# Performance work log

Hardware: AMD Instinct MI355X
Metric: run time of the kernel (lower is better)

## Reference

```python
import jax, jax.numpy as jnp
import numpy as np

B, T, D, V, M, K = 16, 4096, 512, 32000, 256, 3
OPERATOR_RANK = 8
COVERAGE_FLOOR = 0.05
LN_EPS = 1e-5


def _causal_conv(h, w, b):
    # h: [B,T,D] -> NCH layout, left-pad K-1 for causality (matches F.pad((pad,0)))
    x = h.transpose(0, 2, 1)
    k = w.shape[-1]
    y = jax.lax.conv_general_dilated(x, w, (1,), [(k - 1, 0)],
                                     dimension_numbers=('NCH', 'OIH', 'NCH'))
    return (y + b[None, :, None]).transpose(0, 2, 1)


def _layernorm(x, g, b):
    mu = x.mean(-1, keepdims=True)
    var = ((x - mu) ** 2).mean(-1, keepdims=True)
    return (x - mu) * jax.lax.rsqrt(var + LN_EPS) * g + b


def _masked_median(vals, mask):
    # torch .median() on n valid elems = sorted[(n-1)//2] (lower median)
    valid = mask > 0.5
    cnt = valid.sum(-1)  # [B]
    s = jnp.sort(jnp.where(valid, vals, jnp.inf), axis=-1)
    idx = jnp.maximum((cnt - 1) // 2, 0).astype(jnp.int32)
    med = jnp.take_along_axis(s, idx[:, None], axis=-1)  # [B,1]
    return jnp.where(cnt[:, None] > 0, med, 0.0)


def setup_inputs() -> dict:
    key = jax.random.key(0)
    ks = jax.random.split(key, 10)
    return {
        'prompt_content_units': jax.random.randint(ks[0], (B, T), 0, V),
        'prompt_duration_obs': jax.random.uniform(ks[1], (B, T), minval=0.01, maxval=1.0),
        'prompt_mask': (jax.random.uniform(ks[2], (B, T)) < 0.9).astype(jnp.float32),
        'emb': jax.random.normal(ks[3], (V, D)) * 0.02,
        'proj_w': jax.random.normal(ks[4], (D, 4)) * 0.1,
        'proj_b': jnp.zeros((D,)),
        'conv1_w': jax.random.normal(ks[5], (D, D, K)) * 0.02,
        'conv1_b': jnp.zeros((D,)),
        'conv2_w': jax.random.normal(ks[6], (D, D, K)) * 0.02,
        'conv2_b': jnp.zeros((D,)),
        'ln_g': jnp.ones((D,)),
        'ln_b': jnp.zeros((D,)),
        'role_key': jax.random.normal(ks[7], (M, D)) * 0.02,
    }


def reference(prompt_content_units, prompt_duration_obs, prompt_mask,
              emb, proj_w, proj_b, conv1_w, conv1_b, conv2_w, conv2_b,
              ln_g, ln_b, role_key):
    mask = jnp.clip(prompt_mask, 0.0, 1.0)                       # [B,T]
    logdur = jnp.log(jnp.maximum(prompt_duration_obs, 1e-4)) * mask
    z = jnp.zeros_like(logdur)
    aux = jnp.stack([logdur, z, z, z], axis=-1)                  # [B,T,4]
    hidden = emb[prompt_content_units] + aux @ proj_w.T + proj_b # [B,T,D]
    hidden = jax.nn.gelu(_causal_conv(hidden, conv1_w, conv1_b), approximate=False)
    hidden = jax.nn.gelu(_causal_conv(hidden, conv2_w, conv2_b), approximate=False)
    hidden = _layernorm(hidden, ln_g, ln_b) * mask[..., None]

    score = jnp.einsum('btd,md->btm', hidden, role_key) / jnp.sqrt(jnp.float32(D))
    score = jnp.where(mask[..., None] <= 0.0, -10000.0, score)
    attn = jax.nn.softmax(score, axis=-1) * mask[..., None]      # [B,T,M]

    support = jnp.maximum(mask.sum(1, keepdims=True), 1.0)       # [B,1]
    global_rate = _masked_median(logdur, mask)                   # [B,1]
    ref_residual = (logdur - global_rate) * mask                 # [B,T]

    coverage = jnp.maximum(attn.sum(1), 1e-6)                    # [B,M]
    role_value = jnp.einsum('btm,bt->bm', attn, ref_residual) / coverage
    diff2 = (ref_residual[..., None] - role_value[:, None, :]) ** 2
    role_var = jnp.maximum((attn * diff2).sum(1) / coverage, 1e-4)
    role_cov = jnp.maximum(coverage / support, COVERAGE_FLOOR)
    prompt_role_fit = jnp.einsum('btm,bm->bt', attn, role_value) * mask
    zero_operator = jnp.zeros((mask.shape[0], OPERATOR_RANK), dtype=prompt_duration_obs.dtype)

    return (global_rate, zero_operator, role_value, role_var, role_cov,
            mask, logdur, ref_residual, attn, prompt_role_fit)
```

## Files before the change

### kernel.cpp

```cpp
#include <hip/hip_runtime.h>
#include <math.h>
#include <stdint.h>

#define B_  16
#define T_  4096
#define D_  512
#define M_  256
#define TP_ 4098

static constexpr long O_RATE = 0;
static constexpr long O_ZOP  = 16;
static constexpr long O_RVAL = 144;
static constexpr long O_RVAR = 4240;
static constexpr long O_RCOV = 8336;
static constexpr long O_MASK = 12432;
static constexpr long O_LOGD = 77968;
static constexpr long O_RESID= 143504;
static constexpr long O_ATTN = 209040;
static constexpr long O_FIT  = 16986256;

typedef unsigned short u16;
typedef unsigned int u32;
typedef __attribute__((ext_vector_type(8))) __bf16 bf16x8;
typedef __attribute__((ext_vector_type(4))) float fx4;

__device__ __forceinline__ float b2f(u16 u){ union{float f;uint32_t i;}v; v.i=((uint32_t)u)<<16; return v.f; }
__device__ __forceinline__ u16 f2b(float f){ union{float f;uint32_t i;}v; v.f=f; uint32_t r=v.i+0x7fffu+((v.i>>16)&1u); return (u16)(r>>16); }
__device__ __forceinline__ float clip01(float x){ return fminf(fmaxf(x, 0.f), 1.f); }
__device__ __forceinline__ float gelu_f(float x){ return 0.5f*x*(1.0f+erff(x*0.70710678118654752440f)); }

__device__ __forceinline__ void cp16(const u16* g, u16* l){
  __builtin_amdgcn_global_load_lds((__attribute__((address_space(1))) void*)g,
                                   (__attribute__((address_space(3))) void*)l, 16, 0, 0);
}


__global__ void k_init(u16* __restrict__ h0, u16* __restrict__ hA, int Cloc,
                       float* __restrict__ out){
  int i = blockIdx.x*256 + threadIdx.x;
  int nA = Cloc << 7;
  if (i < nA){
    int lb = i >> 7, r = i & 127, g = r >> 1, t = r & 1;
    *(uint4*)(h0 + ((long)(lb*64 + g)*TP_ + t)*8) = make_uint4(0,0,0,0);
  } else if (i < nA + 2048){
    int j = i - nA;
    int b = j >> 7, r = j & 127, g = r >> 1, t = r & 1;
    *(uint4*)(hA + ((long)(b*64 + g)*TP_ + t)*8) = make_uint4(0,0,0,0);
  } else if (i < nA + 2048 + 128){
    out[O_ZOP + (i - nA - 2048)] = 0.f;
  }
}

__global__ void k_repack(const float* __restrict__ w1, const float* __restrict__ w2,
                         const float* __restrict__ rk, const float* __restrict__ lng,
                         u16* __restrict__ wrp2, u16* __restrict__ rkb){
  int i = blockIdx.x*256 + threadIdx.x;
  if (i < 1572864){
    int gi = i >> 3, c7 = i & 7;
    int row = gi & 511;
    int g   = (gi >> 9) & 3;
    int kt  = (gi >> 11) & 15;
    int tg  = gi >> 15;
    int conv = tg / 3, tap = tg % 3;
    int ic = kt*32 + g*8 + c7;
    const float* w = conv ? w2 : w1;
    wrp2[i] = f2b(w[(row*512 + ic)*3 + tap]);
  } else {
    int j = i - 1572864;
    int gi = j >> 3, c7 = j & 7;
    int n  = gi & 255;
    int g  = (gi >> 8) & 3;
    int kt = gi >> 10;
    int k  = kt*32 + g*8 + c7;
    rkb[j] = f2b(rk[n*512 + k] * lng[k]);
  }
}

__global__ __launch_bounds__(64) void k_gbb(const float* __restrict__ rk,
                                            const float* __restrict__ lng,
                                            const float* __restrict__ lnb,
                                            float* __restrict__ GB,
                                            float* __restrict__ BeB){
  int n = blockIdx.x, lane = threadIdx.x;
  float sg = 0.f, sb = 0.f;
  #pragma unroll
  for (int j = 0; j < 8; ++j){
    int k = lane*8 + j;
    float kv = rk[(long)n*512 + k];
    sg += lng[k]*kv; sb += lnb[k]*kv;
  }
  #pragma unroll
  for (int d=1; d<64; d<<=1){ sg += __shfl_xor(sg, d); sb += __shfl_xor(sb, d); }
  if (lane == 0){ GB[n] = sg; BeB[n] = sb; }
}

__global__ __launch_bounds__(1024) void k_median(
    const float* __restrict__ dur, const float* __restrict__ msk,
    float* __restrict__ out, float* __restrict__ supp_f){
  __shared__ u32 keys[4096];
  __shared__ u32 hist[2048];
  __shared__ float sred[1024];
  __shared__ u32 selBin, selRank;
  __shared__ float sMed;
  const int tid = threadIdx.x;
  const int b = blockIdx.x;
  float msum = 0.f;
  for (int i = tid; i < 4096; i += 1024){
    int bt = (b << 12) + i;
    float m  = clip01(msk[bt]);
    float ld = logf(fmaxf(dur[bt], 1e-4f)) * m;
    out[O_MASK + bt] = m;
    out[O_LOGD + bt] = ld;
    u32 u = __float_as_uint(ld);
    u32 k = (u & 0x80000000u) ? ~u : (u | 0x80000000u);
    keys[i] = (m > 0.5f) ? k : 0xFFFFFFFFu;
    msum += m;
  }
  sred[tid] = msum;
  __syncthreads();
  for (int s = 512; s > 0; s >>= 1){
    if (tid < s) sred[tid] += sred[tid + s];
    __syncthreads();
  }
  float msumT = sred[0];
  int cnt = (int)(msumT + 0.5f);
  u32 prefix = 0;
  u32 r = (cnt > 0) ? (u32)((cnt - 1) >> 1) : 0u;
  if (cnt > 0){
    #pragma unroll
    for (int p = 0; p < 3; ++p){
      const int shift = (p==0) ? 21 : (p==1) ? 10 : 0;
      const int nb = (p==2) ? 1024 : 2048;
      const u32 himask = (p==0) ? 0u : (0xFFFFFFFFu << (shift + ((p==2)?10:11)));
      hist[tid] = 0u; hist[tid + 1024] = 0u;
      __syncthreads();
      for (int i = tid; i < 4096; i += 1024){
        u32 k = keys[i];
        if ((k & himask) == prefix)
          atomicAdd(&hist[(k >> shift) & (u32)(nb-1)], 1u);
      }
      __syncthreads();
      if (tid < 64){
        u32 lane = tid;
        u32 cum = 0;
        for (int chunk = 0; chunk < nb/64; ++chunk){
          u32 v = hist[chunk*64 + lane];
          u32 incl = v;
          #pragma unroll
          for (int d = 1; d < 64; d <<= 1){
            u32 o = __shfl_up(incl, d);
            if (lane >= (u32)d) incl += o;
          }
          u32 total = __shfl(incl, 63);
          if (r < cum + total){
            u32 excl = incl - v;
            bool hit = (r >= cum + excl) && (r < cum + excl + v);
            unsigned long long bal = __ballot(hit);
            int L = __ffsll((unsigned long long)bal) - 1;
            u32 exclL = __shfl(excl, L);
            if (lane == 0){ selBin = (u32)(chunk*64 + L); selRank = r - (cum + exclL); }
            break;
          }
          cum += total;
        }
      }
      __syncthreads();
      prefix |= (selBin << shift);
      r = selRank;
      __syncthreads();
    }
  }
  if (tid == 0){
    float med = 0.f;
    if (cnt > 0){
      u32 k = prefix;
      u32 u = (k & 0x80000000u) ? (k ^ 0x80000000u) : ~k;
      med = __uint_as_float(u);
    }
    out[O_RATE + b] = med;
    supp_f[b] = fmaxf(msumT, 1.0f);
    sMed = med;
  }
  __syncthreads();
  float med = sMed;
  for (int i = tid; i < 4096; i += 1024){
    int bt = (b << 12) + i;
    float m  = clip01(msk[bt]);
    float ld = logf(fmaxf(dur[bt], 1e-4f)) * m;
    out[O_RESID + bt] = (ld - med) * m;
  }
}

__global__ __launch_bounds__(256) void k_embed(
    const int* __restrict__ units, const float* __restrict__ dur,
    const float* __restrict__ msk, const float* __restrict__ emb,
    const float* __restrict__ pw, const float* __restrict__ pb,
    u16* __restrict__ h0, int b0){
  int wid = threadIdx.x >> 6, lane = threadIdx.x & 63;
  int w = blockIdx.x*4 + wid;
  int tb = w & 63, g = (w >> 6) & 63, lb = w >> 12;
  int t = tb*64 + lane;
  int bt = ((b0 + lb) << 12) + t;
  float m = clip01(msk[bt]);
  float ld = logf(fmaxf(dur[bt], 1e-4f)) * m;
  long u = units[bt];
  const float* er = emb + u*512 + g*8;
  float4 e0 = *(const float4*)er;
  float4 e1 = *(const float4*)(er + 4);
  float x[8] = {e0.x,e0.y,e0.z,e0.w,e1.x,e1.y,e1.z,e1.w};
  union { u16 s[8]; uint4 v; } o;
  #pragma unroll
  for (int j=0;j<8;++j)
    o.s[j] = f2b(x[j] + ld*pw[(g*8+j)*4] + pb[g*8+j]);
  *(uint4*)(h0 + ((long)(lb*64 + g)*TP_ + 2 + t)*8) = o.v;
}

__device__ __forceinline__ void stageA(u16* smem, const u16* hin, long aG, int t0,
                                       int tid, int kt, int base){
  { int s = tid;
    int gl = s / 258, row = s - gl*258;
    cp16(hin + (aG + (long)(kt*4 + gl)*TP_ + t0 + row)*8, &smem[(base + s)*8]); }
  if (tid < 8){
    int s = 1024 + tid;
    cp16(hin + (aG + (long)(kt*4 + 3)*TP_ + t0 + (s - 774))*8, &smem[(base + s)*8]);
  }
}
__device__ __forceinline__ void stageB(u16* smem, const u16* w, int n0,
                                       int tid, int kt, int base){
  #pragma unroll
  for (int q = 0; q < 3; ++q){
    int s2 = q*1024 + tid;
    int tap = s2 >> 10, g = (s2 >> 8) & 3, col = s2 & 255;
    cp16(w + ((long)((tap*16 + kt)*4 + g)*512 + n0 + col)*8, &smem[(base + s2)*8]);
  }
}

template<int STATS>
__global__ __launch_bounds__(1024, 4) void k_conv(const u16* __restrict__ hin,
                                                  const u16* __restrict__ wrp2c,
                                                  const float* __restrict__ bias,
                                                  u16* __restrict__ hout,
                                                  float* __restrict__ rsum,
                                                  float* __restrict__ rsumsq,
                                                  int statsBase, int nwg){
  __shared__ __align__(16) u16 smem[65664];
  const int tid = threadIdx.x;
  const int lane = tid & 63, wid = tid >> 6;
  const int wm = wid >> 2, wn = wid & 3;
  const int g4 = lane >> 4, r16 = lane & 15;
  const int cpx = nwg >> 3;
  const int wg  = ((int)blockIdx.x & 7)*cpx + ((int)blockIdx.x >> 3);
  const int nt = wg & 1, mt = wg >> 1;
  const int lb = mt >> 4, t0 = (mt & 15) << 8;
  const int n0 = nt << 8;
  const long aG = (long)lb*64*TP_;

  fx4 acc[4][4];
  #pragma unroll
  for (int i=0;i<4;++i)
    #pragma unroll
    for (int j=0;j<4;++j){ acc[i][j][0]=0.f; acc[i][j][1]=0.f; acc[i][j][2]=0.f; acc[i][j][3]=0.f; }

  stageB(smem, wrp2c, n0, tid, 0, 2064);
  stageA(smem, hin, aG, t0, tid, 0, 0);

  int cur = 0;
  #pragma unroll 1
  for (int kt = 0; kt < 16; ++kt){
    if (kt < 15){
      stageB(smem, wrp2c, n0, tid, kt+1, 2064 + (cur^1)*3072);
      stageA(smem, hin, aG, t0, tid, kt+1, (cur^1)*1032);
      asm volatile("s_waitcnt vmcnt(4)" ::: "memory");
    } else {
      asm volatile("s_waitcnt vmcnt(0)" ::: "memory");
    }
    __builtin_amdgcn_s_barrier();
    __builtin_amdgcn_sched_barrier(0);
    {
      const u16* Ab = &smem[cur*1032*8];
      const u16* Bb = &smem[(2064 + cur*3072)*8];
      #pragma unroll
      for (int tap = 0; tap < 3; ++tap){
        bf16x8 af[4], bf[4];
        #pragma unroll
        for (int mi=0;mi<4;++mi)
          af[mi] = *(const bf16x8*)&Ab[(g4*258 + wm*64 + mi*16 + r16 + tap)*8];
        #pragma unroll
        for (int ni=0;ni<4;++ni)
          bf[ni] = *(const bf16x8*)&Bb[(tap*1024 + g4*256 + wn*64 + ni*16 + r16)*8];
        __builtin_amdgcn_s_setprio(1);
        #pragma unroll
        for (int mi=0;mi<4;++mi)
          #pragma unroll
          for (int ni=0;ni<4;++ni)
            acc[mi][ni] = __builtin_amdgcn_mfma_f32_16x16x32_bf16(af[mi], bf[ni], acc[mi][ni], 0,0,0);
        __builtin_amdgcn_s_setprio(0);
      }
    }
    __builtin_amdgcn_sched_barrier(0);
    __builtin_amdgcn_s_barrier();
    cur ^= 1;
  }

  __builtin_amdgcn_sched_barrier(0);
  const int cl = r16;
  float bv[4];
  #pragma unroll
  for (int ni=0;ni<4;++ni) bv[ni] = bias[n0 + wn*64 + ni*16 + cl];
  #pragma unroll
  for (int mi=0;mi<4;++mi)
    #pragma unroll
    for (int rg=0;rg<4;++rg){
      int r = wm*64 + mi*16 + g4*4 + rg;
      float sv = 0.f, sv2 = 0.f;
      #pragma unroll
      for (int ni=0;ni<4;++ni){
        float v = gelu_f(acc[mi][ni][rg] + bv[ni]);
        int c = wn*64 + ni*16 + cl;
        smem[(c >> 3)*2048 + r*8 + (c & 7)] = f2b(v);
        if (STATS){ sv += v; sv2 += v*v; }
      }
      if (STATS){
        #pragma unroll
        for (int d=1; d<16; d<<=1){ sv += __shfl_xor(sv, d); sv2 += __shfl_xor(sv2, d); }
        if (cl == 0){
          int grow = statsBase + lb*4096 + t0 + r;
          atomicAdd(&rsum[grow], sv);
          atomicAdd(&rsumsq[grow], sv2);
        }
      }
    }
  __syncthreads();
  #pragma unroll
  for (int it = 0; it < 8; ++it){
    int s = it*1024 + tid;
    int gc = s >> 8, row = s & 255;
    long gran = aG + (long)(nt*32 + gc)*TP_ + 2 + t0 + row;
    *(uint4*)(hout + gran*8) = *(const uint4*)&smem[gc*2048 + row*8];
  }
}

__global__ __launch_bounds__(512, 4) void k_score(const u16* __restrict__ h,
                                                  const u16* __restrict__ rkb,
                                                  const float* __restrict__ msk,
                                                  const float* __restrict__ rsum,
                                                  const float* __restrict__ rsumsq,
                                                  const float* __restrict__ GB,
                                                  const float* __restrict__ BeB,
                                                  float* __restrict__ S0,
                                                  float* __restrict__ S1,
                                                  float* __restrict__ S2,
                                                  float* __restrict__ out, int b0){
  __shared__ __align__(16) u16 smem[24960];
  __shared__ float smax[128][4];
  __shared__ float ssum[128][4];
  const int tid = threadIdx.x;
  const int lane = tid & 63, wid = tid >> 6;
  const int wm = wid >> 2, wn = wid & 3;
  const int g4 = lane >> 4, r16 = lane & 15;
  const int cpx = (int)gridDim.x >> 3;
  const int wg  = ((int)blockIdx.x & 7)*cpx + ((int)blockIdx.x >> 3);
  const int r0 = wg << 7;
  const int lb = r0 >> 12, t0 = r0 & 4095;
  const int gb = b0 + lb;
  const long gRow0 = ((long)gb << 12) + t0;
  const long aG = (long)lb*64*TP_;

  fx4 acc[4][4];
  #pragma unroll
  for (int i=0;i<4;++i)
    #pragma unroll
    for (int j=0;j<4;++j){ acc[i][j][0]=0.f; acc[i][j][1]=0.f; acc[i][j][2]=0.f; acc[i][j][3]=0.f; }

  #define SC_STAGE(kt, buf) do {                                               \
    int s = tid; int gl = s >> 7, row = s & 127;                               \
    cp16(h + (aG + (long)((kt)*4 + gl)*TP_ + 2 + t0 + row)*8,                  \
         &smem[((buf)*520 + gl*130 + row)*8]);                                 \
    _Pragma("unroll")                                                          \
    for (int q = 0; q < 2; ++q){                                               \
      int s2 = q*512 + tid;                                                    \
      int g = s2 >> 8, col = s2 & 255;                                         \
      cp16(rkb + ((long)(kt)*1024 + s2)*8,                                     \
           &smem[(1040 + (buf)*1040 + g*260 + col)*8]);                        \
    } } while(0)

  SC_STAGE(0, 0);
  #pragma unroll 1
  for (int kt = 0; kt < 16; ++kt){
    const int cur = kt & 1;
    if (kt < 15){
      SC_STAGE(kt+1, cur^1);
      asm volatile("s_waitcnt vmcnt(3)" ::: "memory");
    } else {
      asm volatile("s_waitcnt vmcnt(0)" ::: "memory");
    }
    __builtin_amdgcn_s_barrier();
    __builtin_amdgcn_sched_barrier(0);
    {
      const u16* Ab = &smem[(cur*520)*8];
      const u16* Bb = &smem[(1040 + cur*1040)*8];
      bf16x8 af[4], bf[4];
      #pragma unroll
      for (int mi=0;mi<4;++mi)
        af[mi] = *(const bf16x8*)&Ab[(g4*130 + wm*64 + mi*16 + r16)*8];
      #pragma unroll
      for (int ni=0;ni<4;++ni)
        bf[ni] = *(const bf16x8*)&Bb[(g4*260 + wn*64 + ni*16 + r16)*8];
      __builtin_amdgcn_s_setprio(1);
      #pragma unroll
      for (int mi=0;mi<4;++mi)
        #pragma unroll
        for (int ni=0;ni<4;++ni)
          acc[mi][ni] = __builtin_amdgcn_mfma_f32_16x16x32_bf16(af[mi], bf[ni], acc[mi][ni], 0,0,0);
      __builtin_amdgcn_s_setprio(0);
    }
    __builtin_amdgcn_sched_barrier(0);
    __builtin_amdgcn_s_barrier();
  }
  #undef SC_STAGE

  const float SCALE = 0.044194173824159216f;
  const int cl = r16;
  float gbv[4], bbv[4];
  #pragma unroll
  for (int ni=0;ni<4;++ni){
    int col = wn*64 + ni*16 + cl;
    gbv[ni] = GB[col]; bbv[ni] = BeB[col];
  }
  float gmx[4][4];
  #pragma unroll
  for (int mi=0;mi<4;++mi)
    #pragma unroll
    for (int rg=0;rg<4;++rg){
      int row = wm*64 + mi*16 + g4*4 + rg;
      long gRow = gRow0 + row;
      float mk = clip01(msk[gRow]);
      float mu = rsum[gRow] * (1.f/512.f);
      float var = rsumsq[gRow] * (1.f/512.f) - mu*mu;
      float inv = rsqrtf(var + 1e-5f);
      float mx = -1e30f;
      #pragma unroll
      for (int ni=0;ni<4;++ni){
        float s = mk * SCALE * (inv*(acc[mi][ni][rg] - mu*gbv[ni]) + bbv[ni]);
        acc[mi][ni][rg] = s;
        mx = fmaxf(mx, s);
      }
      #pragma unroll
      for (int d=1; d<16; d<<=1) mx = fmaxf(mx, __shfl_xor(mx, d));
      if (cl == 0) smax[row][wn] = mx;
    }
  __syncthreads();
  #pragma unroll
  for (int mi=0;mi<4;++mi)
    #pragma unroll
    for (int rg=0;rg<4;++rg){
      int row = wm*64 + mi*16 + g4*4 + rg;
      gmx[mi][rg] = fmaxf(fmaxf(smax[row][0], smax[row][1]),
                          fmaxf(smax[row][2], smax[row][3]));
    }
  #pragma unroll
  for (int mi=0;mi<4;++mi)
    #pragma unroll
    for (int rg=0;rg<4;++rg){
      float s = 0.f;
      #pragma unroll
      for (int ni=0;ni<4;++ni){
        float e = expf(acc[mi][ni][rg] - gmx[mi][rg]);
        acc[mi][ni][rg] = e;
        s += e;
      }
      #pragma unroll
      for (int d=1; d<16; d<<=1) s += __shfl_xor(s, d);
      if (cl == 0) ssum[wm*64 + mi*16 + g4*4 + rg][wn] = s;
    }
  __syncthreads();
  float* fbuf = (float*)smem;
  float ps0[4], ps1[4], ps2[4];
  #pragma unroll
  for (int ni=0;ni<4;++ni){ ps0[ni]=0.f; ps1[ni]=0.f; ps2[ni]=0.f; }
  #pragma unroll
  for (int mi=0;mi<4;++mi){
    __syncthreads();
    #pragma unroll
    for (int rg=0;rg<4;++rg){
      int row = wm*64 + mi*16 + g4*4 + rg;
      long gRow = gRow0 + row;
      float tot = (ssum[row][0] + ssum[row][1]) + (ssum[row][2] + ssum[row][3]);
      float mk = clip01(msk[gRow]);
      float f = mk / tot;
      float rr = out[O_RESID + gRow];
      #pragma unroll
      for (int ni=0;ni<4;++ni){
        float a = acc[mi][ni][rg] * f;
        fbuf[(wm*16 + g4*4 + rg)*260 + wn*64 + ni*16 + cl] = a;
        ps0[ni] += a; ps1[ni] += a*rr; ps2[ni] += a*rr*rr;
      }
    }
    __syncthreads();
    #pragma unroll
    for (int p=0;p<4;++p){
      int lrow = p*8 + (tid >> 6);
      int c4 = tid & 63;
      float4 v = *(const float4*)&fbuf[lrow*260 + c4*4];
      int grow = (lrow >> 4)*64 + mi*16 + (lrow & 15);
      *(float4*)(out + O_ATTN + (gRow0 + grow)*M_ + c4*4) = v;
    }
  }
  #pragma unroll
  for (int ni=0;ni<4;++ni){
    ps0[ni] += __shfl_xor(ps0[ni], 16); ps0[ni] += __shfl_xor(ps0[ni], 32);
    ps1[ni] += __shfl_xor(ps1[ni], 16); ps1[ni] += __shfl_xor(ps1[ni], 32);
    ps2[ni] += __shfl_xor(ps2[ni], 16); ps2[ni] += __shfl_xor(ps2[ni], 32);
  }
  if (g4 == 0){
    #pragma unroll
    for (int ni=0;ni<4;++ni){
      int col = wn*64 + ni*16 + cl;
      atomicAdd(&S0[gb*M_ + col], ps0[ni]);
      atomicAdd(&S1[gb*M_ + col], ps1[ni]);
      atomicAdd(&S2[gb*M_ + col], ps2[ni]);
    }
  }
}

__global__ __launch_bounds__(256) void k_final(const float* __restrict__ S0,
                                               const float* __restrict__ S1,
                                               const float* __restrict__ S2,
                                               const float* __restrict__ supp,
                                               float* __restrict__ out,
                                               float* __restrict__ rvf){
  int i = blockIdx.x*256 + threadIdx.x;
  int b = i >> 8;
  float s0 = S0[i], s1 = S1[i], s2 = S2[i];
  float cov = fmaxf(s0, 1e-6f);
  float rv = s1 / cov;
  float var = fmaxf((s2 - 2.f*rv*s1 + rv*rv*s0) / cov, 1e-4f);
  float rc = fmaxf(cov / supp[b], 0.05f);
  out[O_RVAL + i] = rv;
  out[O_RVAR + i] = var;
  out[O_RCOV + i] = rc;
  rvf[i] = rv;
}

__global__ __launch_bounds__(256) void k_fit(const float* __restrict__ attn,
                                             const float* __restrict__ rvf,
                                             const float* __restrict__ msk,
                                             float* __restrict__ out){
  int wid = threadIdx.x >> 6, lane = threadIdx.x & 63;
  int row = blockIdx.x*4 + wid;
  int b = row >> 12;
  float4 a = *(const float4*)(attn + (long)row*M_ + lane*4);
  float4 r = *(const float4*)(rvf + b*M_ + lane*4);
  float dot = a.x*r.x + a.y*r.y + a.z*r.z + a.w*r.w;
  #pragma unroll
  for (int d=1; d<64; d<<=1) dot += __shfl_xor(dot, d);
  if (lane == 0) out[O_FIT + row] = dot * clip01(msk[row]);
}

extern "C" void kernel_launch(void* const* d_in, const int* in_sizes, int n_in,
                              void* d_out, int out_size, void* d_ws, size_t ws_size,
                              hipStream_t stream) {
  const int*   units = (const int*)d_in[0];
  const float* dur   = (const float*)d_in[1];
  const float* msk   = (const float*)d_in[2];
  const float* emb   = (const float*)d_in[3];
  const float* pw    = (const float*)d_in[4];
  const float* pb    = (const float*)d_in[5];
  const float* w1    = (const float*)d_in[6];
  const float* b1    = (const float*)d_in[7];
  const float* w2    = (const float*)d_in[8];
  const float* b2c   = (const float*)d_in[9];
  const float* lng   = (const float*)d_in[10];
  const float* lnb   = (const float*)d_in[11];
  const float* rk    = (const float*)d_in[12];
  float* out = (float*)d_out;
  char* ws = (char*)d_ws;

  u16* hA = (u16*)(out + O_ATTN);

  const size_t perB = (size_t)64*TP_*16;
  const size_t tail = 3145728 + 262144 + 1024 + 1024 + 64 + 16384 + 49152 + 262144 + 262144;
  int C = 16;
  while (C > 1 && ((size_t)C*perB + tail) > ws_size) C >>= 1;
  const int nch = 16 / C;

  char* p = ws;
  u16*   h0    = (u16*)p;            p += (size_t)C*perB;
  u16*   wrp2  = (u16*)p;            p += 3145728;
  u16*   rkb   = (u16*)p;            p += 262144;
  float* GB    = (float*)p;          p += 1024;
  float* BeB   = (float*)p;          p += 1024;
  float* supp_f= (float*)p;          p += 64;
  float* rv_f  = (float*)p;          p += 16384;
  float* S0    = (float*)p;          p += 49152;
  float* S1    = S0 + 4096;
  float* S2    = S1 + 4096;
  float* rsum  = (float*)p;          p += 262144;
  float* rsumsq= (float*)p;          p += 262144;

  hipMemsetAsync(S0, 0, 49152 + 262144 + 262144, stream);
  int initN = (C << 7) + 2048 + 128;
  k_init  <<<(initN + 255)/256, 256, 0, stream>>>(h0, hA, C, out);
  k_repack<<<6656, 256, 0, stream>>>(w1, w2, rk, lng, wrp2, rkb);
  k_gbb   <<<256,   64, 0, stream>>>(rk, lng, lnb, GB, BeB);
  k_median<<<16,  1024, 0, stream>>>(dur, msk, out, supp_f);
  const int nwg = C*32;
  for (int c = 0; c < nch; ++c){
    int b0 = c*C;
    u16* hAc = hA + (size_t)b0*64*TP_*8;
    k_embed  <<<C*1024, 256, 0, stream>>>(units, dur, msk, emb, pw, pb, h0, b0);
    k_conv<0><<<nwg,   1024, 0, stream>>>(h0,  wrp2,           b1,  hAc, rsum, rsumsq, 0,       nwg);
    k_conv<1><<<nwg,   1024, 0, stream>>>(hAc, wrp2 + 786432,  b2c, h0,  rsum, rsumsq, b0*4096, nwg);
    k_score  <<<nwg,    512, 0, stream>>>(h0, rkb, msk, rsum, rsumsq, GB, BeB, S0, S1, S2, out, b0);
  }
  k_final <<<16,    256, 0, stream>>>(S0, S1, S2, supp_f, out, rv_f);
  k_fit   <<<16384, 256, 0, stream>>>(out + O_ATTN, rv_f, msk, out);
}
```

Baseline: 471.8 us.

## Load conv activation fragments directly from global memory instead of LDS staging

The conv GEMM kernel no longer stages the activation (A) tile into shared memory. Each wave now loads its A fragments for the three taps directly from global memory, and only the weight tile stays double-buffered in LDS. This is meant to cut LDS traffic and footprint for A. The cost is redundant global loads across waves and across the overlapping taps, a full vmcnt(0) wait each iteration, and the loss of the sched_barrier-separated prefetch pipelining.

```diff
diff --git a/kernel.cpp b/kernel.cpp
--- a/kernel.cpp
+++ b/kernel.cpp
@@ -215,16 +215,6 @@
   *(uint4*)(h0 + ((long)(lb*64 + g)*TP_ + 2 + t)*8) = o.v;
 }
 
-__device__ __forceinline__ void stageA(u16* smem, const u16* hin, long aG, int t0,
-                                       int tid, int kt, int base){
-  { int s = tid;
-    int gl = s / 258, row = s - gl*258;
-    cp16(hin + (aG + (long)(kt*4 + gl)*TP_ + t0 + row)*8, &smem[(base + s)*8]); }
-  if (tid < 8){
-    int s = 1024 + tid;
-    cp16(hin + (aG + (long)(kt*4 + 3)*TP_ + t0 + (s - 774))*8, &smem[(base + s)*8]);
-  }
-}
 __device__ __forceinline__ void stageB(u16* smem, const u16* w, int n0,
                                        int tid, int kt, int base){
   #pragma unroll
@@ -243,7 +233,7 @@
                                                   float* __restrict__ rsum,
                                                   float* __restrict__ rsumsq,
                                                   int statsBase, int nwg){
-  __shared__ __align__(16) u16 smem[65664];
+  __shared__ __align__(16) u16 smem[65536];
   const int tid = threadIdx.x;
   const int lane = tid & 63, wid = tid >> 6;
   const int wm = wid >> 2, wn = wid & 3;
@@ -261,45 +251,54 @@
     #pragma unroll
     for (int j=0;j<4;++j){ acc[i][j][0]=0.f; acc[i][j][1]=0.f; acc[i][j][2]=0.f; acc[i][j][3]=0.f; }
 
-  stageB(smem, wrp2c, n0, tid, 0, 2064);
-  stageA(smem, hin, aG, t0, tid, 0, 0);
-
-  int cur = 0;
+  const u16* pA0 = hin + (aG + (long)g4*TP_ + t0 + wm*64 + r16)*8;
+
+  stageB(smem, wrp2c, n0, tid, 0, 0);
+  asm volatile("s_waitcnt vmcnt(0)" ::: "memory");
+  __builtin_amdgcn_s_barrier();
+
   #pragma unroll 1
   for (int kt = 0; kt < 16; ++kt){
-    if (kt < 15){
-      stageB(smem, wrp2c, n0, tid, kt+1, 2064 + (cur^1)*3072);
-      stageA(smem, hin, aG, t0, tid, kt+1, (cur^1)*1032);
-      asm volatile("s_waitcnt vmcnt(4)" ::: "memory");
-    } else {
-      asm volatile("s_waitcnt vmcnt(0)" ::: "memory");
-    }
+    const int cur = kt & 1;
+    const u16* Bb = &smem[(cur*3072)*8];
+    const u16* pAk = pA0 + (long)kt*4*TP_*8;
+    if (kt < 15) stageB(smem, wrp2c, n0, tid, kt+1, (cur^1)*3072);
+    bf16x8 a[4], bf[4];
+    #pragma unroll
+    for (int mi=0;mi<4;++mi) a[mi]  = *(const bf16x8*)(pAk + mi*128);
+    #pragma unroll
+    for (int ni=0;ni<4;++ni) bf[ni] = *(const bf16x8*)&Bb[(g4*256 + wn*64 + ni*16 + r16)*8];
+    __builtin_amdgcn_s_setprio(1);
+    #pragma unroll
+    for (int mi=0;mi<4;++mi)
+      #pragma unroll
+      for (int ni=0;ni<4;++ni)
+        acc[mi][ni] = __builtin_amdgcn_mfma_f32_16x16x32_bf16(a[mi], bf[ni], acc[mi][ni], 0,0,0);
+    __builtin_amdgcn_s_setprio(0);
+    #pragma unroll
+    for (int mi=0;mi<4;++mi) a[mi]  = *(const bf16x8*)(pAk + 8 + mi*128);
+    #pragma unroll
+    for (int ni=0;ni<4;++ni) bf[ni] = *(const bf16x8*)&Bb[(1024 + g4*256 + wn*64 + ni*16 + r16)*8];
+    __builtin_amdgcn_s_setprio(1);
+    #pragma unroll
+    for (int mi=0;mi<4;++mi)
+      #pragma unroll
+      for (int ni=0;ni<4;++ni)
+        acc[mi][ni] = __builtin_amdgcn_mfma_f32_16x16x32_bf16(a[mi], bf[ni], acc[mi][ni], 0,0,0);
+    __builtin_amdgcn_s_setprio(0);
+    #pragma unroll
+    for (int mi=0;mi<4;++mi) a[mi]  = *(const bf16x8*)(pAk + 16 + mi*128);
+    #pragma unroll
+    for (int ni=0;ni<4;++ni) bf[ni] = *(const bf16x8*)&Bb[(2048 + g4*256 + wn*64 + ni*16 + r16)*8];
+    __builtin_amdgcn_s_setprio(1);
+    #pragma unroll
+    for (int mi=0;mi<4;++mi)
+      #pragma unroll
+      for (int ni=0;ni<4;++ni)
+        acc[mi][ni] = __builtin_amdgcn_mfma_f32_16x16x32_bf16(a[mi], bf[ni], acc[mi][ni], 0,0,0);
+    __builtin_amdgcn_s_setprio(0);
+    asm volatile("s_waitcnt vmcnt(0)" ::: "memory");
     __builtin_amdgcn_s_barrier();
-    __builtin_amdgcn_sched_barrier(0);
-    {
-      const u16* Ab = &smem[cur*1032*8];
-      const u16* Bb = &smem[(2064 + cur*3072)*8];
-      #pragma unroll
-      for (int tap = 0; tap < 3; ++tap){
-        bf16x8 af[4], bf[4];
-        #pragma unroll
-        for (int mi=0;mi<4;++mi)
-          af[mi] = *(const bf16x8*)&Ab[(g4*258 + wm*64 + mi*16 + r16 + tap)*8];
-        #pragma unroll
-        for (int ni=0;ni<4;++ni)
-          bf[ni] = *(const bf16x8*)&Bb[(tap*1024 + g4*256 + wn*64 + ni*16 + r16)*8];
-        __builtin_amdgcn_s_setprio(1);
-        #pragma unroll
-        for (int mi=0;mi<4;++mi)
-          #pragma unroll
-          for (int ni=0;ni<4;++ni)
-            acc[mi][ni] = __builtin_amdgcn_mfma_f32_16x16x32_bf16(af[mi], bf[ni], acc[mi][ni], 0,0,0);
-        __builtin_amdgcn_s_setprio(0);
-      }
-    }
-    __builtin_amdgcn_sched_barrier(0);
-    __builtin_amdgcn_s_barrier();
-    cur ^= 1;
   }
 
   __builtin_amdgcn_sched_barrier(0);
```

New measurement: 477.7 us. Within noise of the previous version (+1.3%).
